# Optimization experiments

Hardware: AMD Instinct MI355X
Metric: run time of the kernel (lower is better)

## Reference

```python
import jax, jax.numpy as jnp
import numpy as np

N, E, D = 100000, 640000, 128  # nodes, edges, feature dim (in_dim == out_dim == 128)
BN_EPS = 1e-5


def setup_inputs() -> dict:
    key = jax.random.key(0)
    ks = jax.random.split(key, 8)
    x = jax.random.normal(ks[0], (N, D), dtype=jnp.float32)
    edge_index = jax.random.randint(ks[1], (2, E), 0, N, dtype=jnp.int64)
    s = 1.0 / np.sqrt(D)
    W1 = jax.random.uniform(ks[2], (D, D), jnp.float32, -s, s)
    b1 = jax.random.uniform(ks[3], (D,), jnp.float32, -s, s)
    W2 = jax.random.uniform(ks[4], (D, D), jnp.float32, -s, s)
    b2 = jax.random.uniform(ks[5], (D,), jnp.float32, -s, s)
    return {
        "x": x,
        "edge_index": edge_index,
        "eps": jnp.array([0.1], dtype=jnp.float32),
        "W1": W1, "b1": b1,
        "g1": jnp.ones((D,), jnp.float32), "beta1": jnp.zeros((D,), jnp.float32),
        "W2": W2, "b2": b2,
        "g2": jnp.ones((D,), jnp.float32), "beta2": jnp.zeros((D,), jnp.float32),
    }


def _batchnorm(h, gamma, beta):
    # BatchNorm1d in training mode: biased batch stats over the node dim
    mean = jnp.mean(h, axis=0)
    var = jnp.var(h, axis=0)
    return gamma * (h - mean) * jax.lax.rsqrt(var + BN_EPS) + beta


def reference(x, edge_index, eps, W1, b1, g1, beta1, W2, b2, g2, beta2):
    src, dst = edge_index[0], edge_index[1]
    # gather messages from source nodes, scatter-add into destination nodes
    aggr = jax.ops.segment_sum(x[src], dst, num_segments=x.shape[0])  # [N, D]
    h = (1.0 + eps) * x + aggr
    h = jax.nn.relu(_batchnorm(h @ W1.T + b1, g1, beta1))
    h = jax.nn.relu(_batchnorm(h @ W2.T + b2, g2, beta2))
    return h
```

## Files before the change

### kernel.cpp

```cpp
#include <hip/hip_runtime.h>

#define NN 100000
#define DD 128
#define EE 640000
#define NPAD 100352

typedef __bf16 bf16x8 __attribute__((ext_vector_type(8)));
typedef float floatx4 __attribute__((ext_vector_type(4)));

__device__ __forceinline__ unsigned short f2bf(float f) {
    unsigned int u = __float_as_uint(f);
    u += 0x7FFF + ((u >> 16) & 1);
    return (unsigned short)(u >> 16);
}

__global__ __launch_bounds__(256) void hist_k(const int* __restrict__ ei,
                                              int* __restrict__ deg) {
    int e = blockIdx.x * 256 + threadIdx.x;
    if (e < EE) atomicAdd(&deg[ei[EE + e]], 1);
}

__global__ __launch_bounds__(256) void scan1_k(const int* __restrict__ deg,
                                               int* __restrict__ exc,
                                               int* __restrict__ chunkSums) {
    __shared__ int s[256];
    int t = threadIdx.x, g = blockIdx.x * 256 + t;
    int v = (g < NN) ? deg[g] : 0;
    s[t] = v;
    __syncthreads();
    for (int off = 1; off < 256; off <<= 1) {
        int u = (t >= off) ? s[t - off] : 0;
        __syncthreads();
        s[t] += u;
        __syncthreads();
    }
    if (g < NN) exc[g] = s[t] - v;
    if (t == 255) chunkSums[blockIdx.x] = s[255];
}

__global__ __launch_bounds__(512) void scan2_k(int* __restrict__ chunkSums, int n) {
    __shared__ int s[512];
    int t = threadIdx.x;
    int v = (t < n) ? chunkSums[t] : 0;
    s[t] = v;
    __syncthreads();
    for (int off = 1; off < 512; off <<= 1) {
        int u = (t >= off) ? s[t - off] : 0;
        __syncthreads();
        s[t] += u;
        __syncthreads();
    }
    if (t < n) chunkSums[t] = s[t] - v;
}

__global__ __launch_bounds__(256) void scan3_k(int* __restrict__ exc,
                                               const int* __restrict__ chunkSums,
                                               int* __restrict__ cursor) {
    int g = blockIdx.x * 256 + threadIdx.x;
    if (g < NN) {
        int o = exc[g] + chunkSums[blockIdx.x];
        exc[g] = o;
        cursor[g] = o;
    }
}

__global__ __launch_bounds__(256) void esort_k(const int* __restrict__ ei,
                                               int* __restrict__ cursor,
                                               int* __restrict__ ssrc) {
    int e = blockIdx.x * 256 + threadIdx.x;
    if (e >= EE) return;
    int pos = atomicAdd(&cursor[ei[EE + e]], 1);
    ssrc[pos] = ei[e];
}

__global__ __launch_bounds__(256) void aggregate_k(
    const float4* __restrict__ x4, const int* __restrict__ ssrc,
    const int* __restrict__ offs, const int* __restrict__ deg,
    const float* __restrict__ epsp, ushort4* __restrict__ hout) {
    int tid = blockIdx.x * 256 + threadIdx.x;
    int node = tid >> 5, lane = tid & 31;
    if (node >= NN) return;
    int start = offs[node], d = deg[node];
    float ef = 1.0f + epsp[0];
    float4 v = x4[node * 32 + lane];
    float4 acc = make_float4(ef * v.x, ef * v.y, ef * v.z, ef * v.w);
    for (int j = 0; j < d; ++j) {
        int s = ssrc[start + j];
        float4 xv = x4[s * 32 + lane];
        acc.x += xv.x; acc.y += xv.y; acc.z += xv.z; acc.w += xv.w;
    }
    ushort4 u;
    u.x = f2bf(acc.x); u.y = f2bf(acc.y); u.z = f2bf(acc.z); u.w = f2bf(acc.w);
    hout[node * 32 + lane] = u;
}

__global__ __launch_bounds__(256, 2) void gin_gemm_k(
    const unsigned short* __restrict__ hin,
    const float* __restrict__ W, const float* __restrict__ bias,
    float* __restrict__ y, float* __restrict__ stats) {
    __shared__ __align__(16) unsigned short Ah[128][136];
    __shared__ __align__(16) unsigned short Bw[128][136];
    __shared__ __align__(16) float s_sum[128];
    __shared__ __align__(16) float s_sq[128];

    const int tid = threadIdx.x;
    const int rowBase = blockIdx.x * 128;

    if (tid < 128) { s_sum[tid] = 0.f; s_sq[tid] = 0.f; }

    const float4* W4 = (const float4*)W;
#pragma unroll
    for (int j = 0; j < 16; ++j) {
        int f4 = j * 256 + tid;
        int row = f4 >> 5, k4 = f4 & 31;
        float4 wv = W4[f4];
        ushort4 u;
        u.x = f2bf(wv.x); u.y = f2bf(wv.y); u.z = f2bf(wv.z); u.w = f2bf(wv.w);
        *(ushort4*)&Bw[row][k4 * 4] = u;
    }

    const int4* h16 = (const int4*)hin;
#pragma unroll
    for (int j = 0; j < 8; ++j) {
        int c = j * 256 + tid;
        int row = c >> 4, c8 = c & 15;
        int rg = rowBase + row;
        int4 v = make_int4(0, 0, 0, 0);
        if (rg < NN) v = h16[rg * 16 + c8];
        *(int4*)&Ah[row][c8 * 8] = v;
    }

    __syncthreads();

    const int l = tid & 63, w = tid >> 6;
    const int m = l & 15, q = l >> 4;

    floatx4 acc[2][8];
#pragma unroll
    for (int rt = 0; rt < 2; ++rt)
#pragma unroll
        for (int ct = 0; ct < 8; ++ct) acc[rt][ct] = (floatx4)0.0f;

#pragma unroll
    for (int kc = 0; kc < 4; ++kc) {
        int k0 = kc * 32 + q * 8;
        bf16x8 a0 = *(const bf16x8*)&Ah[w * 32 + m][k0];
        bf16x8 a1 = *(const bf16x8*)&Ah[w * 32 + 16 + m][k0];
#pragma unroll
        for (int ct = 0; ct < 8; ++ct) {
            bf16x8 b = *(const bf16x8*)&Bw[ct * 16 + m][k0];
            acc[0][ct] = __builtin_amdgcn_mfma_f32_16x16x32_bf16(a0, b, acc[0][ct], 0, 0, 0);
            acc[1][ct] = __builtin_amdgcn_mfma_f32_16x16x32_bf16(a1, b, acc[1][ct], 0, 0, 0);
        }
    }

#pragma unroll
    for (int ct = 0; ct < 8; ++ct) {
        int col = ct * 16 + m;
        float bc = bias[col];
        float ps = 0.f, pq = 0.f;
#pragma unroll
        for (int rt = 0; rt < 2; ++rt) {
#pragma unroll
            for (int i = 0; i < 4; ++i) {
                int rg = rowBase + w * 32 + rt * 16 + q * 4 + i;
                if (rg < NN) {
                    float yv = acc[rt][ct][i] + bc;
                    y[rg * 128 + col] = yv;
                    ps += yv;
                    pq += yv * yv;
                }
            }
        }
        atomicAdd(&s_sum[col], ps);
        atomicAdd(&s_sq[col], pq);
    }
    __syncthreads();
    if (tid < 128) {
        unsafeAtomicAdd(&stats[tid], s_sum[tid]);
        unsafeAtomicAdd(&stats[128 + tid], s_sq[tid]);
    }
}

template <int OUT_BF16>
__global__ __launch_bounds__(256) void bn_relu_k(
    const float* __restrict__ y, const float* __restrict__ stats,
    const float* __restrict__ g, const float* __restrict__ beta,
    float* outf, unsigned short* __restrict__ outh) {
    __shared__ __align__(16) float sc[128];
    __shared__ __align__(16) float sh[128];
    int t = threadIdx.x;
    if (t < 128) {
        const float inv = 1.0f / (float)NN;
        float mean = stats[t] * inv;
        float var = stats[128 + t] * inv - mean * mean;
        float s = g[t] * rsqrtf(var + 1e-5f);
        sc[t] = s;
        sh[t] = beta[t] - mean * s;
    }
    __syncthreads();
    const int total4 = NN * 32;
    const float4* y4 = (const float4*)y;
    for (int i = blockIdx.x * 256 + t; i < total4; i += gridDim.x * 256) {
        int c4 = i & 31;
        float4 v = y4[i];
        float4 s = ((const float4*)sc)[c4];
        float4 b = ((const float4*)sh)[c4];
        float r0 = fmaxf(v.x * s.x + b.x, 0.f);
        float r1 = fmaxf(v.y * s.y + b.y, 0.f);
        float r2 = fmaxf(v.z * s.z + b.z, 0.f);
        float r3 = fmaxf(v.w * s.w + b.w, 0.f);
        if (OUT_BF16) {
            ushort4 u;
            u.x = f2bf(r0); u.y = f2bf(r1); u.z = f2bf(r2); u.w = f2bf(r3);
            ((ushort4*)outh)[i] = u;
        } else {
            ((float4*)outf)[i] = make_float4(r0, r1, r2, r3);
        }
    }
}

extern "C" void kernel_launch(void* const* d_in, const int* in_sizes, int n_in,
                              void* d_out, int out_size, void* d_ws, size_t ws_size,
                              hipStream_t stream) {
    const float* x   = (const float*)d_in[0];
    const int* ei    = (const int*)d_in[1];
    const float* W1  = (const float*)d_in[3];
    const float* b1  = (const float*)d_in[4];
    const float* g1  = (const float*)d_in[5];
    const float* be1 = (const float*)d_in[6];
    const float* W2  = (const float*)d_in[7];
    const float* b2  = (const float*)d_in[8];
    const float* g2  = (const float*)d_in[9];
    const float* be2 = (const float*)d_in[10];
    const float* eps = (const float*)d_in[2];
    float* out = (float*)d_out;

    int* deg        = (int*)d_ws;
    int* offs       = deg + NPAD;
    int* cursor     = offs + NPAD;
    int* chunkSums  = cursor + NPAD;
    int* ssrc       = chunkSums + 512;
    unsigned short* hbuf = (unsigned short*)(ssrc + EE + 256);
    float* stats    = (float*)(hbuf + (size_t)NN * DD);

    hipMemsetAsync(deg, 0, NPAD * sizeof(int), stream);
    hipMemsetAsync(stats, 0, 512 * sizeof(float), stream);

    const int numChunks = (NN + 255) / 256;
    hist_k<<<(EE + 255) / 256, 256, 0, stream>>>(ei, deg);
    scan1_k<<<numChunks, 256, 0, stream>>>(deg, offs, chunkSums);
    scan2_k<<<1, 512, 0, stream>>>(chunkSums, numChunks);
    scan3_k<<<numChunks, 256, 0, stream>>>(offs, chunkSums, cursor);
    esort_k<<<(EE + 255) / 256, 256, 0, stream>>>(ei, cursor, ssrc);
    aggregate_k<<<(NN * 32 + 255) / 256, 256, 0, stream>>>(
        (const float4*)x, ssrc, offs, deg, eps, (ushort4*)hbuf);

    int gblocks = (NN + 127) / 128;
    gin_gemm_k<<<gblocks, 256, 0, stream>>>(hbuf, W1, b1, out, stats);
    bn_relu_k<1><<<4096, 256, 0, stream>>>(out, stats, g1, be1, nullptr, hbuf);
    gin_gemm_k<<<gblocks, 256, 0, stream>>>(hbuf, W2, b2, out, stats + 256);
    bn_relu_k<0><<<4096, 256, 0, stream>>>(out, stats + 256, g2, be2, out, nullptr);
}
```

Measured before the change: 359.8 us.

## Gather bf16 features, fuse BN1+ReLU into second GEMM, merge preprocessing kernels

A single pre-kernel now builds the degree histogram and converts x, W1 and W2 to bf16. The x copy is staged in the output buffer so the neighbour gather reads half the bytes, with 16 lanes per node each loading 8 values. The first BatchNorm+ReLU is applied while the second GEMM loads its A operand from fp32 y, which removes a full elementwise pass and the bf16 intermediate. The GEMMs now read operands straight from global memory instead of staging them in LDS, and the stats memset and the offs array are folded into the scan kernels. In exchange, neighbour features are summed at bf16 precision, and the second GEMM reads the BN scale and shift from LDS on every A-fragment load.

```diff
diff --git a/kernel.cpp b/kernel.cpp
--- a/kernel.cpp
+++ b/kernel.cpp
@@ -4,9 +4,12 @@
 #define DD 128
 #define EE 640000
 #define NPAD 100352
+#define NCHUNK 391
 
 typedef __bf16 bf16x8 __attribute__((ext_vector_type(8)));
 typedef float floatx4 __attribute__((ext_vector_type(4)));
+
+union FragU { int4 i; bf16x8 b; unsigned short us[8]; };
 
 __device__ __forceinline__ unsigned short f2bf(float f) {
     unsigned int u = __float_as_uint(f);
@@ -14,14 +17,39 @@
     return (unsigned short)(u >> 16);
 }
 
-__global__ __launch_bounds__(256) void hist_k(const int* __restrict__ ei,
-                                              int* __restrict__ deg) {
-    int e = blockIdx.x * 256 + threadIdx.x;
-    if (e < EE) atomicAdd(&deg[ei[EE + e]], 1);
+#define HBLK 2500
+#define XBLK 3200
+__global__ __launch_bounds__(256) void pre_k(
+    const int* __restrict__ ei, int* __restrict__ deg,
+    const float4* __restrict__ x4, ushort4* __restrict__ xb4,
+    const float4* __restrict__ W1, const float4* __restrict__ W2,
+    ushort4* __restrict__ wb1, ushort4* __restrict__ wb2) {
+    int bid = blockIdx.x;
+    if (bid < HBLK) {
+        int e = bid * 256 + threadIdx.x;
+        atomicAdd(&deg[ei[EE + e]], 1);
+    } else if (bid < HBLK + XBLK) {
+        for (int i = (bid - HBLK) * 256 + threadIdx.x; i < NN * 32;
+             i += XBLK * 256) {
+            float4 v = x4[i];
+            ushort4 u;
+            u.x = f2bf(v.x); u.y = f2bf(v.y); u.z = f2bf(v.z); u.w = f2bf(v.w);
+            xb4[i] = u;
+        }
+    } else {
+        int wb = bid - HBLK - XBLK;
+        const float4* src = (wb < 16) ? W1 : W2;
+        ushort4* dst = (wb < 16) ? wb1 : wb2;
+        int i = (wb & 15) * 256 + threadIdx.x;
+        float4 v = src[i];
+        ushort4 u;
+        u.x = f2bf(v.x); u.y = f2bf(v.y); u.z = f2bf(v.z); u.w = f2bf(v.w);
+        dst[i] = u;
+    }
 }
 
 __global__ __launch_bounds__(256) void scan1_k(const int* __restrict__ deg,
-                                               int* __restrict__ exc,
+                                               int* __restrict__ cursor,
                                                int* __restrict__ chunkSums) {
     __shared__ int s[256];
     int t = threadIdx.x, g = blockIdx.x * 256 + t;
@@ -34,13 +62,15 @@
         s[t] += u;
         __syncthreads();
     }
-    if (g < NN) exc[g] = s[t] - v;
+    if (g < NN) cursor[g] = s[t] - v;
     if (t == 255) chunkSums[blockIdx.x] = s[255];
 }
 
-__global__ __launch_bounds__(512) void scan2_k(int* __restrict__ chunkSums, int n) {
+__global__ __launch_bounds__(512) void scan2_k(int* __restrict__ chunkSums,
+                                               int n, float* __restrict__ stats) {
     __shared__ int s[512];
     int t = threadIdx.x;
+    stats[t] = 0.f;
     int v = (t < n) ? chunkSums[t] : 0;
     s[t] = v;
     __syncthreads();
@@ -53,15 +83,10 @@
     if (t < n) chunkSums[t] = s[t] - v;
 }
 
-__global__ __launch_bounds__(256) void scan3_k(int* __restrict__ exc,
-                                               const int* __restrict__ chunkSums,
-                                               int* __restrict__ cursor) {
+__global__ __launch_bounds__(256) void scan3_k(int* __restrict__ cursor,
+                                               const int* __restrict__ chunkSums) {
     int g = blockIdx.x * 256 + threadIdx.x;
-    if (g < NN) {
-        int o = exc[g] + chunkSums[blockIdx.x];
-        exc[g] = o;
-        cursor[g] = o;
-    }
+    if (g < NN) cursor[g] += chunkSums[blockIdx.x];
 }
 
 __global__ __launch_bounds__(256) void esort_k(const int* __restrict__ ei,
@@ -74,64 +99,64 @@
 }
 
 __global__ __launch_bounds__(256) void aggregate_k(
-    const float4* __restrict__ x4, const int* __restrict__ ssrc,
-    const int* __restrict__ offs, const int* __restrict__ deg,
-    const float* __restrict__ epsp, ushort4* __restrict__ hout) {
+    const float* __restrict__ x, const unsigned short* __restrict__ xb,
+    const int* __restrict__ ssrc, const int* __restrict__ cursor,
+    const int* __restrict__ deg, const float* __restrict__ epsp,
+    unsigned short* __restrict__ hout) {
     int tid = blockIdx.x * 256 + threadIdx.x;
-    int node = tid >> 5, lane = tid & 31;
+    int node = tid >> 4, lane = tid & 15;
     if (node >= NN) return;
-    int start = offs[node], d = deg[node];
+    int d = deg[node];
+    int start = cursor[node] - d;
     float ef = 1.0f + epsp[0];
-    float4 v = x4[node * 32 + lane];
-    float4 acc = make_float4(ef * v.x, ef * v.y, ef * v.z, ef * v.w);
+
+    const float4* xs = (const float4*)(x + node * 128 + lane * 8);
+    float4 s0 = xs[0], s1 = xs[1];
+    float acc[8] = {ef * s0.x, ef * s0.y, ef * s0.z, ef * s0.w,
+                    ef * s1.x, ef * s1.y, ef * s1.z, ef * s1.w};
+
     for (int j = 0; j < d; ++j) {
         int s = ssrc[start + j];
-        float4 xv = x4[s * 32 + lane];
-        acc.x += xv.x; acc.y += xv.y; acc.z += xv.z; acc.w += xv.w;
-    }
-    ushort4 u;
-    u.x = f2bf(acc.x); u.y = f2bf(acc.y); u.z = f2bf(acc.z); u.w = f2bf(acc.w);
-    hout[node * 32 + lane] = u;
-}
-
-__global__ __launch_bounds__(256, 2) void gin_gemm_k(
-    const unsigned short* __restrict__ hin,
-    const float* __restrict__ W, const float* __restrict__ bias,
-    float* __restrict__ y, float* __restrict__ stats) {
-    __shared__ __align__(16) unsigned short Ah[128][136];
-    __shared__ __align__(16) unsigned short Bw[128][136];
-    __shared__ __align__(16) float s_sum[128];
-    __shared__ __align__(16) float s_sq[128];
-
+        int4 raw = *(const int4*)(xb + s * 128 + lane * 8);
+        unsigned int u0 = (unsigned int)raw.x, u1 = (unsigned int)raw.y;
+        unsigned int u2 = (unsigned int)raw.z, u3 = (unsigned int)raw.w;
+        acc[0] += __uint_as_float(u0 << 16);
+        acc[1] += __uint_as_float(u0 & 0xffff0000u);
+        acc[2] += __uint_as_float(u1 << 16);
+        acc[3] += __uint_as_float(u1 & 0xffff0000u);
+        acc[4] += __uint_as_float(u2 << 16);
+        acc[5] += __uint_as_float(u2 & 0xffff0000u);
+        acc[6] += __uint_as_float(u3 << 16);
+        acc[7] += __uint_as_float(u3 & 0xffff0000u);
+    }
+    FragU o;
+#pragma unroll
+    for (int i = 0; i < 8; ++i) o.us[i] = f2bf(acc[i]);
+    *(int4*)(hout + node * 128 + lane * 8) = o.i;
+}
+
+template <int MODE>
+__global__ __launch_bounds__(256) void gemm_k(
+    const unsigned short* __restrict__ hA,
+    float* y,
+    const unsigned short* __restrict__ Wb, const float* __restrict__ bias,
+    const float* __restrict__ stats_in, const float* __restrict__ g,
+    const float* __restrict__ be, float* __restrict__ stats_out) {
+    __shared__ float sc[128], sh[128];
+    __shared__ float s_sum[128], s_sq[128];
     const int tid = threadIdx.x;
+    if (tid < 128) { s_sum[tid] = 0.f; s_sq[tid] = 0.f; }
+    if (MODE == 1 && tid < 128) {
+        const float inv = 1.0f / (float)NN;
+        float mean = stats_in[tid] * inv;
+        float var = stats_in[128 + tid] * inv - mean * mean;
+        float s = g[tid] * rsqrtf(var + 1e-5f);
+        sc[tid] = s;
+        sh[tid] = be[tid] - mean * s;
+    }
+    __syncthreads();
+
     const int rowBase = blockIdx.x * 128;
-
-    if (tid < 128) { s_sum[tid] = 0.f; s_sq[tid] = 0.f; }
-
-    const float4* W4 = (const float4*)W;
-#pragma unroll
-    for (int j = 0; j < 16; ++j) {
-        int f4 = j * 256 + tid;
-        int row = f4 >> 5, k4 = f4 & 31;
-        float4 wv = W4[f4];
-        ushort4 u;
-        u.x = f2bf(wv.x); u.y = f2bf(wv.y); u.z = f2bf(wv.z); u.w = f2bf(wv.w);
-        *(ushort4*)&Bw[row][k4 * 4] = u;
-    }
-
-    const int4* h16 = (const int4*)hin;
-#pragma unroll
-    for (int j = 0; j < 8; ++j) {
-        int c = j * 256 + tid;
-        int row = c >> 4, c8 = c & 15;
-        int rg = rowBase + row;
-        int4 v = make_int4(0, 0, 0, 0);
-        if (rg < NN) v = h16[rg * 16 + c8];
-        *(int4*)&Ah[row][c8 * 8] = v;
-    }
-
-    __syncthreads();
-
     const int l = tid & 63, w = tid >> 6;
     const int m = l & 15, q = l >> 4;
 
@@ -141,16 +166,40 @@
 #pragma unroll
         for (int ct = 0; ct < 8; ++ct) acc[rt][ct] = (floatx4)0.0f;
 
-#pragma unroll
+#pragma unroll 1
     for (int kc = 0; kc < 4; ++kc) {
-        int k0 = kc * 32 + q * 8;
-        bf16x8 a0 = *(const bf16x8*)&Ah[w * 32 + m][k0];
-        bf16x8 a1 = *(const bf16x8*)&Ah[w * 32 + 16 + m][k0];
+        const int k0 = kc * 32 + q * 8;
+        bf16x8 a[2];
+#pragma unroll
+        for (int rt = 0; rt < 2; ++rt) {
+            int rg = rowBase + w * 32 + rt * 16 + m;
+            FragU u;
+            if (MODE == 0) {
+                u.i = (rg < NN) ? *(const int4*)(hA + rg * 128 + k0)
+                                : make_int4(0, 0, 0, 0);
+            } else {
+                if (rg < NN) {
+                    const float4* p = (const float4*)(y + rg * 128 + k0);
+                    float4 v0 = p[0], v1 = p[1];
+                    u.us[0] = f2bf(fmaxf(v0.x * sc[k0+0] + sh[k0+0], 0.f));
+                    u.us[1] = f2bf(fmaxf(v0.y * sc[k0+1] + sh[k0+1], 0.f));
+                    u.us[2] = f2bf(fmaxf(v0.z * sc[k0+2] + sh[k0+2], 0.f));
+                    u.us[3] = f2bf(fmaxf(v0.w * sc[k0+3] + sh[k0+3], 0.f));
+                    u.us[4] = f2bf(fmaxf(v1.x * sc[k0+4] + sh[k0+4], 0.f));
+                    u.us[5] = f2bf(fmaxf(v1.y * sc[k0+5] + sh[k0+5], 0.f));
+                    u.us[6] = f2bf(fmaxf(v1.z * sc[k0+6] + sh[k0+6], 0.f));
+                    u.us[7] = f2bf(fmaxf(v1.w * sc[k0+7] + sh[k0+7], 0.f));
+                } else {
+                    u.i = make_int4(0, 0, 0, 0);
+                }
+            }
+            a[rt] = u.b;
+        }
 #pragma unroll
         for (int ct = 0; ct < 8; ++ct) {
-            bf16x8 b = *(const bf16x8*)&Bw[ct * 16 + m][k0];
-            acc[0][ct] = __builtin_amdgcn_mfma_f32_16x16x32_bf16(a0, b, acc[0][ct], 0, 0, 0);
-            acc[1][ct] = __builtin_amdgcn_mfma_f32_16x16x32_bf16(a1, b, acc[1][ct], 0, 0, 0);
+            bf16x8 b = *(const bf16x8*)(Wb + (ct * 16 + m) * 128 + k0);
+            acc[0][ct] = __builtin_amdgcn_mfma_f32_16x16x32_bf16(a[0], b, acc[0][ct], 0, 0, 0);
+            acc[1][ct] = __builtin_amdgcn_mfma_f32_16x16x32_bf16(a[1], b, acc[1][ct], 0, 0, 0);
         }
     }
 
@@ -177,16 +226,14 @@
     }
     __syncthreads();
     if (tid < 128) {
-        unsafeAtomicAdd(&stats[tid], s_sum[tid]);
-        unsafeAtomicAdd(&stats[128 + tid], s_sq[tid]);
-    }
-}
-
-template <int OUT_BF16>
-__global__ __launch_bounds__(256) void bn_relu_k(
-    const float* __restrict__ y, const float* __restrict__ stats,
-    const float* __restrict__ g, const float* __restrict__ beta,
-    float* outf, unsigned short* __restrict__ outh) {
+        unsafeAtomicAdd(&stats_out[tid], s_sum[tid]);
+        unsafeAtomicAdd(&stats_out[128 + tid], s_sq[tid]);
+    }
+}
+
+__global__ __launch_bounds__(256) void bn_final_k(
+    float* y, const float* __restrict__ stats,
+    const float* __restrict__ g, const float* __restrict__ beta) {
     __shared__ __align__(16) float sc[128];
     __shared__ __align__(16) float sh[128];
     int t = threadIdx.x;
@@ -200,23 +247,17 @@
     }
     __syncthreads();
     const int total4 = NN * 32;
-    const float4* y4 = (const float4*)y;
+    float4* y4 = (float4*)y;
     for (int i = blockIdx.x * 256 + t; i < total4; i += gridDim.x * 256) {
         int c4 = i & 31;
         float4 v = y4[i];
         float4 s = ((const float4*)sc)[c4];
         float4 b = ((const float4*)sh)[c4];
-        float r0 = fmaxf(v.x * s.x + b.x, 0.f);
-        float r1 = fmaxf(v.y * s.y + b.y, 0.f);
-        float r2 = fmaxf(v.z * s.z + b.z, 0.f);
-        float r3 = fmaxf(v.w * s.w + b.w, 0.f);
-        if (OUT_BF16) {
-            ushort4 u;
-            u.x = f2bf(r0); u.y = f2bf(r1); u.z = f2bf(r2); u.w = f2bf(r3);
-            ((ushort4*)outh)[i] = u;
-        } else {
-            ((float4*)outf)[i] = make_float4(r0, r1, r2, r3);
-        }
+        v.x = fmaxf(v.x * s.x + b.x, 0.f);
+        v.y = fmaxf(v.y * s.y + b.y, 0.f);
+        v.z = fmaxf(v.z * s.z + b.z, 0.f);
+        v.w = fmaxf(v.w * s.w + b.w, 0.f);
+        y4[i] = v;
     }
 }
 
@@ -225,6 +266,7 @@
                               hipStream_t stream) {
     const float* x   = (const float*)d_in[0];
     const int* ei    = (const int*)d_in[1];
+    const float* eps = (const float*)d_in[2];
     const float* W1  = (const float*)d_in[3];
     const float* b1  = (const float*)d_in[4];
     const float* g1  = (const float*)d_in[5];
@@ -233,32 +275,34 @@
     const float* b2  = (const float*)d_in[8];
     const float* g2  = (const float*)d_in[9];
     const float* be2 = (const float*)d_in[10];
-    const float* eps = (const float*)d_in[2];
     float* out = (float*)d_out;
 
     int* deg        = (int*)d_ws;
-    int* offs       = deg + NPAD;
-    int* cursor     = offs + NPAD;
+    int* cursor     = deg + NPAD;
     int* chunkSums  = cursor + NPAD;
     int* ssrc       = chunkSums + 512;
-    unsigned short* hbuf = (unsigned short*)(ssrc + EE + 256);
-    float* stats    = (float*)(hbuf + (size_t)NN * DD);
+    unsigned short* hbuf = (unsigned short*)(ssrc + EE);
+    unsigned short* wb1  = hbuf + (size_t)NN * DD;
+    unsigned short* wb2  = wb1 + 16384;
+    float* stats    = (float*)(wb2 + 16384);
+    unsigned short* xb = (unsigned short*)d_out;
 
     hipMemsetAsync(deg, 0, NPAD * sizeof(int), stream);
-    hipMemsetAsync(stats, 0, 512 * sizeof(float), stream);
-
-    const int numChunks = (NN + 255) / 256;
-    hist_k<<<(EE + 255) / 256, 256, 0, stream>>>(ei, deg);
-    scan1_k<<<numChunks, 256, 0, stream>>>(deg, offs, chunkSums);
-    scan2_k<<<1, 512, 0, stream>>>(chunkSums, numChunks);
-    scan3_k<<<numChunks, 256, 0, stream>>>(offs, chunkSums, cursor);
+
+    pre_k<<<HBLK + XBLK + 32, 256, 0, stream>>>(
+        ei, deg, (const float4*)x, (ushort4*)xb,
+        (const float4*)W1, (const float4*)W2, (ushort4*)wb1, (ushort4*)wb2);
+    scan1_k<<<NCHUNK, 256, 0, stream>>>(deg, cursor, chunkSums);
+    scan2_k<<<1, 512, 0, stream>>>(chunkSums, NCHUNK, stats);
+    scan3_k<<<NCHUNK, 256, 0, stream>>>(cursor, chunkSums);
     esort_k<<<(EE + 255) / 256, 256, 0, stream>>>(ei, cursor, ssrc);
-    aggregate_k<<<(NN * 32 + 255) / 256, 256, 0, stream>>>(
-        (const float4*)x, ssrc, offs, deg, eps, (ushort4*)hbuf);
-
-    int gblocks = (NN + 127) / 128;
-    gin_gemm_k<<<gblocks, 256, 0, stream>>>(hbuf, W1, b1, out, stats);
-    bn_relu_k<1><<<4096, 256, 0, stream>>>(out, stats, g1, be1, nullptr, hbuf);
-    gin_gemm_k<<<gblocks, 256, 0, stream>>>(hbuf, W2, b2, out, stats + 256);
-    bn_relu_k<0><<<4096, 256, 0, stream>>>(out, stats + 256, g2, be2, out, nullptr);
-}
+    aggregate_k<<<(NN * 16 + 255) / 256, 256, 0, stream>>>(
+        x, xb, ssrc, cursor, deg, eps, hbuf);
+
+    const int gblocks = (NN + 127) / 128;
+    gemm_k<0><<<gblocks, 256, 0, stream>>>(hbuf, out, wb1, b1,
+                                           nullptr, nullptr, nullptr, stats);
+    gemm_k<1><<<gblocks, 256, 0, stream>>>(nullptr, out, wb2, b2,
+                                           stats, g1, be1, stats + 256);
+    bn_final_k<<<4096, 256, 0, stream>>>(out, stats + 256, g2, be2);
+}
```

Measured after the change: 366.0 us. Within noise of the previous version (+1.7%).
